# Kernel tuning notes

Hardware: AMD Instinct MI355X
Metric: run time of the kernel (lower is better)

## Reference

```python
import jax, jax.numpy as jnp
import numpy as np

B, S, H = 2, 2048, 4096
NH, NKV, HD = 32, 8, 128
N_REP = NH // NKV
SCALING = HD ** -0.5


def rotate_half(x):
    x1, x2 = x[..., : HD // 2], x[..., HD // 2 :]
    return jnp.concatenate((-x2, x1), axis=-1)


def setup_inputs() -> dict:
    key = jax.random.key(0)
    ks = jax.random.split(key, 8)
    hidden_states = jax.random.normal(ks[0], (B, S, H), dtype=jnp.float32)
    # RoPE tables computed as in Llama (deterministic, realistic values)
    inv_freq = 1.0 / (10000.0 ** (jnp.arange(0, HD, 2, dtype=jnp.float32) / HD))
    t = jnp.arange(S, dtype=jnp.float32)
    freqs = jnp.einsum('s,d->sd', t, inv_freq)
    emb = jnp.concatenate((freqs, freqs), axis=-1)  # [S, HD]
    cos = jnp.broadcast_to(jnp.cos(emb)[None], (B, S, HD))
    sin = jnp.broadcast_to(jnp.sin(emb)[None], (B, S, HD))
    # additive causal mask [B,1,S,S]
    causal = jnp.where(jnp.tril(jnp.ones((S, S), dtype=bool)), 0.0, -1e9).astype(jnp.float32)
    attention_mask = jnp.broadcast_to(causal[None, None], (B, 1, S, S))
    std = 0.02
    Wq = jax.random.normal(ks[1], (NH * HD, H), dtype=jnp.float32) * std
    Wk = jax.random.normal(ks[2], (NKV * HD, H), dtype=jnp.float32) * std
    Wv = jax.random.normal(ks[3], (NKV * HD, H), dtype=jnp.float32) * std
    Wo = jax.random.normal(ks[4], (H, NH * HD), dtype=jnp.float32) * std
    return dict(hidden_states=hidden_states, cos=cos, sin=sin,
                attention_mask=attention_mask, Wq=Wq, Wk=Wk, Wv=Wv, Wo=Wo)


def reference(hidden_states, cos, sin, attention_mask, Wq, Wk, Wv, Wo):
    b, s, _ = hidden_states.shape
    # projections (torch Linear: x @ W.T), split into heads -> [B, nH, S, HD]
    q = (hidden_states @ Wq.T).reshape(b, s, NH, HD).transpose(0, 2, 1, 3)
    k = (hidden_states @ Wk.T).reshape(b, s, NKV, HD).transpose(0, 2, 1, 3)
    v = (hidden_states @ Wv.T).reshape(b, s, NKV, HD).transpose(0, 2, 1, 3)
    # RoPE: cos/sin [B,S,HD] -> [B,1,S,HD]
    c, sn = cos[:, None], sin[:, None]
    q = q * c + rotate_half(q) * sn
    k = k * c + rotate_half(k) * sn
    # GQA: repeat kv heads
    k = jnp.repeat(k, N_REP, axis=1)
    v = jnp.repeat(v, N_REP, axis=1)
    scores = jnp.einsum('bhqd,bhkd->bhqk', q, k) * SCALING + attention_mask
    attn = jax.nn.softmax(scores.astype(jnp.float32), axis=-1).astype(q.dtype)
    out = jnp.einsum('bhqk,bhkd->bhqd', attn, v)
    out = out.transpose(0, 2, 1, 3).reshape(b, s, NH * HD)
    return out @ Wo.T
```

## Files before the change

kernel.cpp:

```cpp
#include <hip/hip_runtime.h>
#include <stdint.h>

typedef unsigned short u16;
typedef __attribute__((ext_vector_type(8))) short short8;
typedef __attribute__((ext_vector_type(4))) float f32x4;
typedef __attribute__((ext_vector_type(16))) float f32x16;
typedef __attribute__((ext_vector_type(4))) u16 u16x4;

static constexpr float SCALE = 0.08838834764831845f;
static constexpr float QSCALE = 0.12752459769642898f;

__device__ __forceinline__ u16 f2bf(float f) {
    union { float f; unsigned u; } x; x.f = f;
    unsigned r = x.u + 0x7fffu + ((x.u >> 16) & 1u);
    return (u16)(r >> 16);
}
__device__ __forceinline__ float bf2f(u16 b) {
    union { unsigned u; float f; } x; x.u = ((unsigned)b) << 16;
    return x.f;
}
__device__ __forceinline__ unsigned cvt_pk_bf16(float lo, float hi_) {
    unsigned r;
    asm("v_cvt_pk_bf16_f32 %0, %1, %2" : "=v"(r) : "v"(lo), "v"(hi_));
    return r;
}

__global__ __launch_bounds__(256) void convert5_kernel(const float* __restrict__ s0, const float* __restrict__ s1,
                                                       const float* __restrict__ s2, const float* __restrict__ s3,
                                                       const float* __restrict__ s4,
                                                       u16* __restrict__ d0, u16* __restrict__ d1,
                                                       u16* __restrict__ d2, u16* __restrict__ d3,
                                                       u16* __restrict__ d4) {
    const int V0 = 4194304, V1 = 8388608, V2 = 9437184, V3 = 10485760, V4 = 14680064;
    const int stride = gridDim.x * blockDim.x;
    for (int i = blockIdx.x * blockDim.x + threadIdx.x; i < V4; i += stride) {
        const float* sp; u16* dp; int off;
        if (i < V0)      { sp = s0; dp = d0; off = i; }
        else if (i < V1) { sp = s1; dp = d1; off = i - V0; }
        else if (i < V2) { sp = s2; dp = d2; off = i - V1; }
        else if (i < V3) { sp = s3; dp = d3; off = i - V2; }
        else             { sp = s4; dp = d4; off = i - V3; }
        float4 v = *reinterpret_cast<const float4*>(sp + (size_t)off * 4);
        u16x4 o;
        o.x = f2bf(v.x); o.y = f2bf(v.y); o.z = f2bf(v.z); o.w = f2bf(v.w);
        *reinterpret_cast<u16x4*>(dp + (size_t)off * 4) = o;
    }
}

__global__ __launch_bounds__(256) void gemm_kv(const u16* __restrict__ A,
                                               const u16* __restrict__ Bk,
                                               const u16* __restrict__ Bv,
                                               u16* __restrict__ Ck,
                                               u16* __restrict__ Cvt) {
    constexpr int K = 4096, N = 1024, BK = 64;
    __shared__ u16 sA[128 * BK];
    __shared__ u16 sB[128 * BK];
    const int tid = threadIdx.x;
    const int wid = tid >> 6, lane = tid & 63;
    const int lrow = lane & 15, lgrp = lane >> 4;

    int bid = blockIdx.x;
    { const int cpx = 512 >> 3; bid = (bid & 7) * cpx + (bid >> 3); }
    const bool isV = bid >= 256;
    const int b2 = bid & 255;
    const int row0 = (b2 >> 3) * 128, col0 = (b2 & 7) * 128;
    const u16* __restrict__ B = isV ? Bv : Bk;
    const int wr = (wid >> 1) * 64, wc = (wid & 1) * 64;

    f32x4 acc[4][4] = {};

    const int NT = K / BK;
    for (int kt = 0; kt < NT; ++kt) {
        const int k0 = kt * BK;
        __syncthreads();
        #pragma unroll
        for (int rnd = 0; rnd < 4; ++rnd) {
            const int eoff = (rnd * 256 + tid) * 8;
            const int r = eoff >> 6, c = eoff & 63;
            const int gc = c ^ ((r & 7) << 3);
            const int ldsoff = rnd * 2048 + wid * 512;
            __builtin_amdgcn_global_load_lds(
                (const __attribute__((address_space(1))) void*)(A + (size_t)(row0 + r) * K + k0 + gc),
                (__attribute__((address_space(3))) void*)(&sA[ldsoff]), 16, 0, 0);
            __builtin_amdgcn_global_load_lds(
                (const __attribute__((address_space(1))) void*)(B + (size_t)(col0 + r) * K + k0 + gc),
                (__attribute__((address_space(3))) void*)(&sB[ldsoff]), 16, 0, 0);
        }
        __syncthreads();
        #pragma unroll
        for (int kk = 0; kk < 2; ++kk) {
            const int koff = kk * 32 + lgrp * 8;
            short8 af[4], bfr[4];
            #pragma unroll
            for (int m = 0; m < 4; ++m) {
                const int rr = wr + m * 16 + lrow;
                af[m] = *(const short8*)&sA[rr * BK + (koff ^ ((rr & 7) << 3))];
            }
            #pragma unroll
            for (int n = 0; n < 4; ++n) {
                const int rr = wc + n * 16 + lrow;
                bfr[n] = *(const short8*)&sB[rr * BK + (koff ^ ((rr & 7) << 3))];
            }
            #pragma unroll
            for (int m = 0; m < 4; ++m)
                #pragma unroll
                for (int n = 0; n < 4; ++n)
                    acc[m][n] = __builtin_amdgcn_mfma_f32_16x16x32_bf16(af[m], bfr[n], acc[m][n], 0, 0, 0);
        }
    }

    const int orow = row0 + wr + lgrp * 4;
    const int ocol = col0 + wc + lrow;
    if (!isV) {
        #pragma unroll
        for (int m = 0; m < 4; ++m)
            #pragma unroll
            for (int n = 0; n < 4; ++n)
                #pragma unroll
                for (int r = 0; r < 4; ++r)
                    Ck[(size_t)(orow + m * 16 + r) * N + ocol + n * 16] = f2bf(acc[m][n][r]);
    } else {
        #pragma unroll
        for (int m = 0; m < 4; ++m)
            #pragma unroll
            for (int n = 0; n < 4; ++n) {
                u16x4 pk;
                pk.x = f2bf(acc[m][n][0]); pk.y = f2bf(acc[m][n][1]);
                pk.z = f2bf(acc[m][n][2]); pk.w = f2bf(acc[m][n][3]);
                *(u16x4*)&Cvt[(size_t)(ocol + n * 16) * 4096 + orow + m * 16] = pk;
            }
    }
}

template<int OUT_MODE>
__global__ __launch_bounds__(512, 1) void gemm256v5(const u16* __restrict__ A,
                                                    const u16* __restrict__ B,
                                                    void* __restrict__ Cv,
                                                    int M, int N, int K) {
    __shared__ u16 sA[2][2][256 * 32];
    __shared__ u16 sB[2][2][256 * 32];
    const int tid = threadIdx.x;
    const int wid = tid >> 6, lane = tid & 63;
    const int lrow = lane & 15, lgrp = lane >> 4;

    const int nbn = N >> 8;
    const int total = (M >> 8) * nbn;
    int bid = blockIdx.x;
    if ((total & 7) == 0) { const int cpx = total >> 3; bid = (bid & 7) * cpx + (bid >> 3); }
    const int row0 = (bid / nbn) * 256, col0 = (bid % nbn) * 256;
    const int wr = (wid >> 2) * 128, wc = (wid & 3) * 64;

    f32x4 acc[8][4] = {};

    const int rS0 = wid * 32 + (lane >> 2);
    const int uS = lane & 3;

    auto stageA = [&](int nb, int kt, int kkh) {
        const int k0 = kt * 64 + kkh * 32;
        #pragma unroll
        for (int g = 0; g < 2; ++g) {
            const int r = rS0 + g * 16;
            const int cs = k0 + ((uS ^ ((r >> 1) & 3)) << 3);
            __builtin_amdgcn_global_load_lds(
                (const __attribute__((address_space(1))) void*)(A + (size_t)(row0 + r) * K + cs),
                (__attribute__((address_space(3))) void*)(&sA[nb][kkh][(wid * 32 + g * 16) * 32]), 16, 0, 0);
        }
    };
    auto stageB = [&](int nb, int kt, int kkh) {
        const int k0 = kt * 64 + kkh * 32;
        #pragma unroll
        for (int g = 0; g < 2; ++g) {
            const int r = rS0 + g * 16;
            const int cs = k0 + ((uS ^ ((r >> 1) & 3)) << 3);
            __builtin_amdgcn_global_load_lds(
                (const __attribute__((address_space(1))) void*)(B + (size_t)(col0 + r) * K + cs),
                (__attribute__((address_space(3))) void*)(&sB[nb][kkh][(wid * 32 + g * 16) * 32]), 16, 0, 0);
        }
    };

    auto rdA = [&](int buf, int kkh, int fr) -> short8 {
        const int r = wr + fr * 16 + lrow;
        return *(const short8*)&sA[buf][kkh][r * 32 + ((lgrp ^ ((r >> 1) & 3)) << 3)];
    };
    auto rdB = [&](int buf, int kkh, int fc) -> short8 {
        const int r = wc + fc * 16 + lrow;
        return *(const short8*)&sB[buf][kkh][r * 32 + ((lgrp ^ ((r >> 1) & 3)) << 3)];
    };

    const int NK = K >> 6;
    stageA(0, 0, 0); stageB(0, 0, 0); stageA(0, 0, 1); stageB(0, 0, 1);
    asm volatile("s_waitcnt vmcnt(4)" ::: "memory");
    __builtin_amdgcn_s_barrier();
    __builtin_amdgcn_sched_barrier(0);

    short8 a0[4], b0[4], a1[4], a2[4], b1[4], a3[4];
    #pragma unroll
    for (int fr = 0; fr < 4; ++fr) a0[fr] = rdA(0, 0, fr);
    #pragma unroll
    for (int fc = 0; fc < 4; ++fc) b0[fc] = rdB(0, 0, fc);
    __builtin_amdgcn_sched_barrier(0);

    for (int kt = 0; kt < NK; ++kt) {
        const int buf = kt & 1, nb = buf ^ 1;
        const bool st = (kt + 1 < NK);

        #pragma unroll
        for (int fr = 0; fr < 4; ++fr) a1[fr] = rdA(buf, 0, fr + 4);
        if (st) stageA(nb, kt + 1, 0);
        asm volatile("s_waitcnt lgkmcnt(4)" ::: "memory");
        __builtin_amdgcn_sched_barrier(0);
        __builtin_amdgcn_s_setprio(1);
        #pragma unroll
        for (int fr = 0; fr < 4; ++fr)
            #pragma unroll
            for (int fc = 0; fc < 4; ++fc)
                acc[fr][fc] = __builtin_amdgcn_mfma_f32_16x16x32_bf16(a0[fr], b0[fc], acc[fr][fc], 0, 0, 0);
        __builtin_amdgcn_s_setprio(0);
        __builtin_amdgcn_sched_barrier(0);

        if (st) stageB(nb, kt + 1, 0);
        asm volatile("s_waitcnt lgkmcnt(0)" ::: "memory");
        __builtin_amdgcn_sched_barrier(0);
        if (st) { asm volatile("s_waitcnt vmcnt(4)" ::: "memory"); }
        else    { asm volatile("s_waitcnt vmcnt(0)" ::: "memory"); }
        __builtin_amdgcn_s_barrier();
        __builtin_amdgcn_sched_barrier(0);
        #pragma unroll
        for (int fr = 0; fr < 4; ++fr) a2[fr] = rdA(buf, 1, fr);
        #pragma unroll
        for (int fc = 0; fc < 4; ++fc) b1[fc] = rdB(buf, 1, fc);
        __builtin_amdgcn_sched_barrier(0);
        __builtin_amdgcn_s_setprio(1);
        #pragma unroll
        for (int fr = 0; fr < 4; ++fr)
            #pragma unroll
            for (int fc = 0; fc < 4; ++fc)
                acc[fr + 4][fc] = __builtin_amdgcn_mfma_f32_16x16x32_bf16(a1[fr], b0[fc], acc[fr + 4][fc], 0, 0, 0);
        __builtin_amdgcn_s_setprio(0);
        __builtin_amdgcn_sched_barrier(0);

        #pragma unroll
        for (int fr = 0; fr < 4; ++fr) a3[fr] = rdA(buf, 1, fr + 4);
        if (st) stageA(nb, kt + 1, 1);
        asm volatile("s_waitcnt lgkmcnt(4)" ::: "memory");
        __builtin_amdgcn_sched_barrier(0);
        __builtin_amdgcn_s_setprio(1);
        #pragma unroll
        for (int fr = 0; fr < 4; ++fr)
            #pragma unroll
            for (int fc = 0; fc < 4; ++fc)
                acc[fr][fc] = __builtin_amdgcn_mfma_f32_16x16x32_bf16(a2[fr], b1[fc], acc[fr][fc], 0, 0, 0);
        __builtin_amdgcn_s_setprio(0);
        __builtin_amdgcn_sched_barrier(0);

        if (st) stageB(nb, kt + 1, 1);
        asm volatile("s_waitcnt lgkmcnt(0)" ::: "memory");
        __builtin_amdgcn_sched_barrier(0);
        if (st) { asm volatile("s_waitcnt vmcnt(4)" ::: "memory"); }
        __builtin_amdgcn_s_barrier();
        __builtin_amdgcn_sched_barrier(0);
        if (st) {
            #pragma unroll
            for (int fr = 0; fr < 4; ++fr) a0[fr] = rdA(nb, 0, fr);
            #pragma unroll
            for (int fc = 0; fc < 4; ++fc) b0[fc] = rdB(nb, 0, fc);
        }
        __builtin_amdgcn_sched_barrier(0);
        __builtin_amdgcn_s_setprio(1);
        #pragma unroll
        for (int fr = 0; fr < 4; ++fr)
            #pragma unroll
            for (int fc = 0; fc < 4; ++fc)
                acc[fr + 4][fc] = __builtin_amdgcn_mfma_f32_16x16x32_bf16(a3[fr], b1[fc], acc[fr + 4][fc], 0, 0, 0);
        __builtin_amdgcn_s_setprio(0);
        __builtin_amdgcn_sched_barrier(0);
    }

    const int orow = row0 + wr + lgrp * 4;
    const int ocol = col0 + wc + lrow;
    if (OUT_MODE == 2) {
        float* C = (float*)Cv;
        #pragma unroll
        for (int m = 0; m < 8; ++m)
            #pragma unroll
            for (int n = 0; n < 4; ++n)
                #pragma unroll
                for (int r = 0; r < 4; ++r)
                    C[(size_t)(orow + m * 16 + r) * N + ocol + n * 16] = acc[m][n][r];
    } else {
        u16* C = (u16*)Cv;
        #pragma unroll
        for (int m = 0; m < 8; ++m)
            #pragma unroll
            for (int n = 0; n < 4; ++n)
                #pragma unroll
                for (int r = 0; r < 4; ++r)
                    C[(size_t)(orow + m * 16 + r) * N + ocol + n * 16] = f2bf(acc[m][n][r]);
    }
}

template<int NHEADS>
__global__ __launch_bounds__(256) void rope_kernel(u16* __restrict__ X,
                                                   const float* __restrict__ cosb,
                                                   const float* __restrict__ sinb,
                                                   float scale) {
    constexpr int LH = (NHEADS == 32) ? 5 : 3;
    const int total = 2 * 2048 * NHEADS * 64;
    const int stride = gridDim.x * blockDim.x;
    for (int i = blockIdx.x * blockDim.x + threadIdx.x; i < total; i += stride) {
        const int d = i & 63;
        const int h = (i >> 6) & (NHEADS - 1);
        const int rs = i >> (6 + LH);
        const size_t base = (size_t)rs * (NHEADS * 128) + h * 128 + d;
        const float c = cosb[rs * 128 + d] * scale;
        const float sn = sinb[rs * 128 + d] * scale;
        const float x1 = bf2f(X[base]);
        const float x2 = bf2f(X[base + 64]);
        X[base] = f2bf(x1 * c - x2 * sn);
        X[base + 64] = f2bf(x2 * c + x1 * sn);
    }
}

__global__ __launch_bounds__(512, 2) void attn_kernel(const u16* __restrict__ Q,
                                                      const u16* __restrict__ K,
                                                      const u16* __restrict__ Vt,
                                                      u16* __restrict__ AO,
                                                      const float* __restrict__ cosp,
                                                      const float* __restrict__ sinp) {
    __shared__ u16 sK[2][64 * 128];
    __shared__ u16 sV[2][128 * 64];
    const int tid = threadIdx.x;
    const int wid = tid >> 6, lane = tid & 63;
    const int l31 = lane & 31, hi = lane >> 5;

    const int gg = blockIdx.x >> 6;
    const int bx = (gg < 4) ? gg : 11 - gg;
    const int rem = blockIdx.x & 63;
    const int h = rem >> 1;
    const int b = rem & 1;
    const int hkv = h >> 2;
    const int rs0 = b * 2048;
    const int q0 = bx * 256;
    const int qw = q0 + wid * 32;
    const int q_lane = qw + l31;

    short8 qf[8];
    {
        const u16* qb = Q + (size_t)(rs0 + q_lane) * 4096 + h * 128 + hi * 8;
        #pragma unroll
        for (int f = 0; f < 8; ++f) qf[f] = *(const short8*)(qb + f * 16);
        const float* cb = cosp + (size_t)(rs0 + q_lane) * 128 + hi * 8;
        const float* sb = sinp + (size_t)(rs0 + q_lane) * 128 + hi * 8;
        #pragma unroll
        for (int f = 0; f < 4; ++f) {
            float4 c0 = *(const float4*)(cb + f * 16);
            float4 c1 = *(const float4*)(cb + f * 16 + 4);
            float4 s0 = *(const float4*)(sb + f * 16);
            float4 s1 = *(const float4*)(sb + f * 16 + 4);
            const float cc[8] = {c0.x, c0.y, c0.z, c0.w, c1.x, c1.y, c1.z, c1.w};
            const float ss[8] = {s0.x, s0.y, s0.z, s0.w, s1.x, s1.y, s1.z, s1.w};
            #pragma unroll
            for (int jj = 0; jj < 8; ++jj) {
                const float x1 = bf2f((u16)qf[f][jj]);
                const float x2 = bf2f((u16)qf[f + 4][jj]);
                qf[f][jj]     = (short)f2bf((x1 * cc[jj] - x2 * ss[jj]) * QSCALE);
                qf[f + 4][jj] = (short)f2bf((x2 * cc[jj] + x1 * ss[jj]) * QSCALE);
            }
        }
    }

    f32x16 accO[4] = {};
    float m_c = -1e30f, l_c = 0.f;

    auto stage = [&](int bf, int t) {
        const int kv0 = t * 64;
        #pragma unroll
        for (int rnd = 0; rnd < 2; ++rnd) {
            {
                const int e = rnd * 4096 + tid * 8;
                const int r = e >> 7, c = e & 127;
                const int cs = c ^ ((r & 15) << 3);
                __builtin_amdgcn_global_load_lds(
                    (const __attribute__((address_space(1))) void*)(K + (size_t)(rs0 + kv0 + r) * 1024 + hkv * 128 + cs),
                    (__attribute__((address_space(3))) void*)(&sK[bf][rnd * 4096 + wid * 512]), 16, 0, 0);
            }
            {
                const int e = rnd * 4096 + tid * 8;
                const int r = e >> 6, c = e & 63;
                const int cs = c ^ ((r & 7) << 3);
                __builtin_amdgcn_global_load_lds(
                    (const __attribute__((address_space(1))) void*)(Vt + (size_t)(hkv * 128 + r) * 4096 + rs0 + kv0 + cs),
                    (__attribute__((address_space(3))) void*)(&sV[bf][rnd * 4096 + wid * 512]), 16, 0, 0);
            }
        }
    };

    const int NT = 4 * (bx + 1);
    stage(0, 0);
    __syncthreads();
    int buf = 0;

    for (int t = 0; t < NT; ++t) {
        if (t + 1 < NT) stage(buf ^ 1, t + 1);
        const int kv0 = t * 64;

        if (kv0 <= qw + 31) {
            f32x16 sc[2] = {};
            #pragma unroll
            for (int f = 0; f < 8; ++f) {
                const int col = f * 16 + hi * 8;
                const int r0 = l31, r1 = 32 + l31;
                short8 k0 = *(const short8*)&sK[buf][r0 * 128 + (col ^ ((r0 & 15) << 3))];
                short8 k1 = *(const short8*)&sK[buf][r1 * 128 + (col ^ ((r1 & 15) << 3))];
                sc[0] = __builtin_amdgcn_mfma_f32_32x32x16_bf16(k0, qf[f], sc[0], 0, 0, 0);
                sc[1] = __builtin_amdgcn_mfma_f32_32x32x16_bf16(k1, qf[f], sc[1], 0, 0, 0);
            }

            if (kv0 + 63 > q_lane) {
                #pragma unroll
                for (int blk = 0; blk < 2; ++blk)
                    #pragma unroll
                    for (int r = 0; r < 16; ++r) {
                        const int kv_abs = kv0 + blk * 32 + ((r & 3) + 8 * (r >> 2) + 4 * hi);
                        if (kv_abs > q_lane) sc[blk][r] = -1e30f;
                    }
            }

            float mx = sc[0][0];
            #pragma unroll
            for (int blk = 0; blk < 2; ++blk)
                #pragma unroll
                for (int r = 0; r < 16; ++r) mx = fmaxf(mx, sc[blk][r]);
            mx = fmaxf(mx, __shfl_xor(mx, 32));

            if (!__all(mx <= m_c + 8.0f)) {
                const float sclf = __builtin_amdgcn_exp2f(m_c - mx);
                m_c = mx;
                l_c *= sclf;
                float sclq[16];
                #pragma unroll
                for (int r = 0; r < 16; ++r)
                    sclq[r] = __shfl(sclf, (r & 3) + 8 * (r >> 2) + 4 * hi);
                #pragma unroll
                for (int d4 = 0; d4 < 4; ++d4)
                    #pragma unroll
                    for (int r = 0; r < 16; ++r) accO[d4][r] *= sclq[r];
            }
            float ssum = 0.f;
            #pragma unroll
            for (int blk = 0; blk < 2; ++blk)
                #pragma unroll
                for (int r = 0; r < 16; ++r) {
                    const float p = __builtin_amdgcn_exp2f(sc[blk][r] - m_c);
                    sc[blk][r] = p;
                    ssum += p;
                }
            ssum += __shfl_xor(ssum, 32);
            l_c += ssum;

            #pragma unroll
            for (int blk = 0; blk < 2; ++blk) {
                #pragma unroll
                for (int tt = 0; tt < 2; ++tt) {
                    const unsigned cv00 = cvt_pk_bf16(sc[blk][8 * tt + 0], sc[blk][8 * tt + 1]);
                    const unsigned cv01 = cvt_pk_bf16(sc[blk][8 * tt + 2], sc[blk][8 * tt + 3]);
                    const unsigned cv10 = cvt_pk_bf16(sc[blk][8 * tt + 4], sc[blk][8 * tt + 5]);
                    const unsigned cv11 = cvt_pk_bf16(sc[blk][8 * tt + 6], sc[blk][8 * tt + 7]);
                    const unsigned s00 = __shfl_xor(cv00, 32);
                    const unsigned s01 = __shfl_xor(cv01, 32);
                    const unsigned s10 = __shfl_xor(cv10, 32);
                    const unsigned s11 = __shfl_xor(cv11, 32);
                    union { unsigned w[4]; short8 v; } pa;
                    pa.w[0] = hi ? s10 : cv00;
                    pa.w[1] = hi ? s11 : cv01;
                    pa.w[2] = hi ? cv10 : s00;
                    pa.w[3] = hi ? cv11 : s01;
                    const int kvb = blk * 32 + tt * 16 + hi * 8;
                    #pragma unroll
                    for (int d4 = 0; d4 < 4; ++d4) {
                        const int vr = d4 * 32 + l31;
                        short8 vf = *(const short8*)&sV[buf][vr * 64 + (kvb ^ ((vr & 7) << 3))];
                        accO[d4] = __builtin_amdgcn_mfma_f32_32x32x16_bf16(pa.v, vf, accO[d4], 0, 0, 0);
                    }
                }
            }
        }
        __syncthreads();
        buf ^= 1;
    }

    const float invl = 1.0f / l_c;
    float invq[16];
    #pragma unroll
    for (int r = 0; r < 16; ++r)
        invq[r] = __shfl(invl, (r & 3) + 8 * (r >> 2) + 4 * hi);
    #pragma unroll
    for (int d4 = 0; d4 < 4; ++d4)
        #pragma unroll
        for (int r = 0; r < 16; ++r) {
            const int q = qw + (r & 3) + 8 * (r >> 2) + 4 * hi;
            AO[(size_t)(rs0 + q) * 4096 + h * 128 + d4 * 32 + l31] = f2bf(accO[d4][r] * invq[r]);
        }
}

extern "C" void kernel_launch(void* const* d_in, const int* in_sizes, int n_in,
                              void* d_out, int out_size, void* d_ws, size_t ws_size,
                              hipStream_t stream) {
    const float* hs   = (const float*)d_in[0];
    const float* cosp = (const float*)d_in[1];
    const float* sinp = (const float*)d_in[2];
    const float* Wq = (const float*)d_in[4];
    const float* Wk = (const float*)d_in[5];
    const float* Wv = (const float*)d_in[6];
    const float* Wo = (const float*)d_in[7];

    u16* Xb = (u16*)d_out;
    u16* Qb = (u16*)d_out + 16777216;
    char* w = (char*)d_ws;
    u16* Wqb = (u16*)w; w += 33554432;
    u16* Wkb = (u16*)w; w += 8388608;
    u16* Wvb = (u16*)w; w += 8388608;
    u16* Wob = (u16*)w; w += 33554432;
    u16* Kb  = (u16*)w; w += 8388608;
    u16* Vtb = (u16*)w; w += 8388608;
    u16* AOb = (u16*)w; w += 33554432;

    convert5_kernel<<<4096, 256, 0, stream>>>(hs, Wq, Wk, Wv, Wo, Xb, Wqb, Wkb, Wvb, Wob);

    gemm256v5<0><<<256, 512, 0, stream>>>(Xb, Wqb, Qb, 4096, 4096, 4096);
    gemm_kv<<<512, 256, 0, stream>>>(Xb, Wkb, Wvb, Kb, Vtb);

    rope_kernel<8><<<1024, 256, 0, stream>>>(Kb, cosp, sinp, 1.0f);

    attn_kernel<<<512, 512, 0, stream>>>(Qb, Kb, Vtb, AOb, cosp, sinp);

    gemm256v5<2><<<256, 512, 0, stream>>>(AOb, Wob, (float*)d_out, 4096, 4096, 4096);
}
```

Measured before the change: 502.4 us.

## Load K and V fragments directly from global memory, dropping LDS staging

The attention kernel no longer stages K and Vt tiles into double-buffered shared memory with async global-to-LDS loads and block barriers. Each wave now reads its MFMA operand fragments straight from global memory and skips fully masked tiles per wave with continue. This removes the LDS traffic, the barriers and the shared-memory footprint. In exchange, the 8 waves of a block each re-read the same K/V data through the cache with no software prefetch, so load latency is exposed.

```diff
diff --git a/kernel.cpp b/kernel.cpp
--- a/kernel.cpp
+++ b/kernel.cpp
@@ -327,8 +327,6 @@
                                                       u16* __restrict__ AO,
                                                       const float* __restrict__ cosp,
                                                       const float* __restrict__ sinp) {
-    __shared__ u16 sK[2][64 * 128];
-    __shared__ u16 sV[2][128 * 64];
     const int tid = threadIdx.x;
     const int wid = tid >> 6, lane = tid & 63;
     const int l31 = lane & 31, hi = lane >> 5;
@@ -372,121 +370,91 @@
     f32x16 accO[4] = {};
     float m_c = -1e30f, l_c = 0.f;
 
-    auto stage = [&](int bf, int t) {
+    const u16* __restrict__ Kb0 = K + (size_t)(rs0 + l31) * 1024 + hkv * 128 + hi * 8;
+    const u16* __restrict__ Kb1 = K + (size_t)(rs0 + 32 + l31) * 1024 + hkv * 128 + hi * 8;
+    const u16* __restrict__ Vb = Vt + (size_t)(hkv * 128 + l31) * 4096 + rs0 + hi * 8;
+
+    const int NT = 4 * (bx + 1);
+    for (int t = 0; t < NT; ++t) {
         const int kv0 = t * 64;
-        #pragma unroll
-        for (int rnd = 0; rnd < 2; ++rnd) {
-            {
-                const int e = rnd * 4096 + tid * 8;
-                const int r = e >> 7, c = e & 127;
-                const int cs = c ^ ((r & 15) << 3);
-                __builtin_amdgcn_global_load_lds(
-                    (const __attribute__((address_space(1))) void*)(K + (size_t)(rs0 + kv0 + r) * 1024 + hkv * 128 + cs),
-                    (__attribute__((address_space(3))) void*)(&sK[bf][rnd * 4096 + wid * 512]), 16, 0, 0);
+        if (kv0 > qw + 31) continue;
+
+        f32x16 sc[2] = {};
+        #pragma unroll
+        for (int f = 0; f < 8; ++f) {
+            short8 k0 = *(const short8*)(Kb0 + (size_t)kv0 * 1024 + f * 16);
+            short8 k1 = *(const short8*)(Kb1 + (size_t)kv0 * 1024 + f * 16);
+            sc[0] = __builtin_amdgcn_mfma_f32_32x32x16_bf16(k0, qf[f], sc[0], 0, 0, 0);
+            sc[1] = __builtin_amdgcn_mfma_f32_32x32x16_bf16(k1, qf[f], sc[1], 0, 0, 0);
+        }
+
+        if (kv0 + 63 > q_lane) {
+            #pragma unroll
+            for (int blk = 0; blk < 2; ++blk)
+                #pragma unroll
+                for (int r = 0; r < 16; ++r) {
+                    const int kv_abs = kv0 + blk * 32 + ((r & 3) + 8 * (r >> 2) + 4 * hi);
+                    if (kv_abs > q_lane) sc[blk][r] = -1e30f;
+                }
+        }
+
+        float mx = sc[0][0];
+        #pragma unroll
+        for (int blk = 0; blk < 2; ++blk)
+            #pragma unroll
+            for (int r = 0; r < 16; ++r) mx = fmaxf(mx, sc[blk][r]);
+        mx = fmaxf(mx, __shfl_xor(mx, 32));
+
+        if (!__all(mx <= m_c + 8.0f)) {
+            const float sclf = __builtin_amdgcn_exp2f(m_c - mx);
+            m_c = mx;
+            l_c *= sclf;
+            float sclq[16];
+            #pragma unroll
+            for (int r = 0; r < 16; ++r)
+                sclq[r] = __shfl(sclf, (r & 3) + 8 * (r >> 2) + 4 * hi);
+            #pragma unroll
+            for (int d4 = 0; d4 < 4; ++d4)
+                #pragma unroll
+                for (int r = 0; r < 16; ++r) accO[d4][r] *= sclq[r];
+        }
+        float ssum = 0.f;
+        #pragma unroll
+        for (int blk = 0; blk < 2; ++blk)
+            #pragma unroll
+            for (int r = 0; r < 16; ++r) {
+                const float p = __builtin_amdgcn_exp2f(sc[blk][r] - m_c);
+                sc[blk][r] = p;
+                ssum += p;
             }
-            {
-                const int e = rnd * 4096 + tid * 8;
-                const int r = e >> 6, c = e & 63;
-                const int cs = c ^ ((r & 7) << 3);
-                __builtin_amdgcn_global_load_lds(
-                    (const __attribute__((address_space(1))) void*)(Vt + (size_t)(hkv * 128 + r) * 4096 + rs0 + kv0 + cs),
-                    (__attribute__((address_space(3))) void*)(&sV[bf][rnd * 4096 + wid * 512]), 16, 0, 0);
-            }
-        }
-    };
-
-    const int NT = 4 * (bx + 1);
-    stage(0, 0);
-    __syncthreads();
-    int buf = 0;
-
-    for (int t = 0; t < NT; ++t) {
-        if (t + 1 < NT) stage(buf ^ 1, t + 1);
-        const int kv0 = t * 64;
-
-        if (kv0 <= qw + 31) {
-            f32x16 sc[2] = {};
-            #pragma unroll
-            for (int f = 0; f < 8; ++f) {
-                const int col = f * 16 + hi * 8;
-                const int r0 = l31, r1 = 32 + l31;
-                short8 k0 = *(const short8*)&sK[buf][r0 * 128 + (col ^ ((r0 & 15) << 3))];
-                short8 k1 = *(const short8*)&sK[buf][r1 * 128 + (col ^ ((r1 & 15) << 3))];
-                sc[0] = __builtin_amdgcn_mfma_f32_32x32x16_bf16(k0, qf[f], sc[0], 0, 0, 0);
-                sc[1] = __builtin_amdgcn_mfma_f32_32x32x16_bf16(k1, qf[f], sc[1], 0, 0, 0);
-            }
-
-            if (kv0 + 63 > q_lane) {
-                #pragma unroll
-                for (int blk = 0; blk < 2; ++blk)
-                    #pragma unroll
-                    for (int r = 0; r < 16; ++r) {
-                        const int kv_abs = kv0 + blk * 32 + ((r & 3) + 8 * (r >> 2) + 4 * hi);
-                        if (kv_abs > q_lane) sc[blk][r] = -1e30f;
-                    }
-            }
-
-            float mx = sc[0][0];
-            #pragma unroll
-            for (int blk = 0; blk < 2; ++blk)
-                #pragma unroll
-                for (int r = 0; r < 16; ++r) mx = fmaxf(mx, sc[blk][r]);
-            mx = fmaxf(mx, __shfl_xor(mx, 32));
-
-            if (!__all(mx <= m_c + 8.0f)) {
-                const float sclf = __builtin_amdgcn_exp2f(m_c - mx);
-                m_c = mx;
-                l_c *= sclf;
-                float sclq[16];
-                #pragma unroll
-                for (int r = 0; r < 16; ++r)
-                    sclq[r] = __shfl(sclf, (r & 3) + 8 * (r >> 2) + 4 * hi);
-                #pragma unroll
-                for (int d4 = 0; d4 < 4; ++d4)
-                    #pragma unroll
-                    for (int r = 0; r < 16; ++r) accO[d4][r] *= sclq[r];
-            }
-            float ssum = 0.f;
-            #pragma unroll
-            for (int blk = 0; blk < 2; ++blk)
-                #pragma unroll
-                for (int r = 0; r < 16; ++r) {
-                    const float p = __builtin_amdgcn_exp2f(sc[blk][r] - m_c);
-                    sc[blk][r] = p;
-                    ssum += p;
-                }
-            ssum += __shfl_xor(ssum, 32);
-            l_c += ssum;
-
-            #pragma unroll
-            for (int blk = 0; blk < 2; ++blk) {
-                #pragma unroll
-                for (int tt = 0; tt < 2; ++tt) {
-                    const unsigned cv00 = cvt_pk_bf16(sc[blk][8 * tt + 0], sc[blk][8 * tt + 1]);
-                    const unsigned cv01 = cvt_pk_bf16(sc[blk][8 * tt + 2], sc[blk][8 * tt + 3]);
-                    const unsigned cv10 = cvt_pk_bf16(sc[blk][8 * tt + 4], sc[blk][8 * tt + 5]);
-                    const unsigned cv11 = cvt_pk_bf16(sc[blk][8 * tt + 6], sc[blk][8 * tt + 7]);
-                    const unsigned s00 = __shfl_xor(cv00, 32);
-                    const unsigned s01 = __shfl_xor(cv01, 32);
-                    const unsigned s10 = __shfl_xor(cv10, 32);
-                    const unsigned s11 = __shfl_xor(cv11, 32);
-                    union { unsigned w[4]; short8 v; } pa;
-                    pa.w[0] = hi ? s10 : cv00;
-                    pa.w[1] = hi ? s11 : cv01;
-                    pa.w[2] = hi ? cv10 : s00;
-                    pa.w[3] = hi ? cv11 : s01;
-                    const int kvb = blk * 32 + tt * 16 + hi * 8;
-                    #pragma unroll
-                    for (int d4 = 0; d4 < 4; ++d4) {
-                        const int vr = d4 * 32 + l31;
-                        short8 vf = *(const short8*)&sV[buf][vr * 64 + (kvb ^ ((vr & 7) << 3))];
-                        accO[d4] = __builtin_amdgcn_mfma_f32_32x32x16_bf16(pa.v, vf, accO[d4], 0, 0, 0);
-                    }
+        ssum += __shfl_xor(ssum, 32);
+        l_c += ssum;
+
+        #pragma unroll
+        for (int blk = 0; blk < 2; ++blk) {
+            #pragma unroll
+            for (int tt = 0; tt < 2; ++tt) {
+                const unsigned cv00 = cvt_pk_bf16(sc[blk][8 * tt + 0], sc[blk][8 * tt + 1]);
+                const unsigned cv01 = cvt_pk_bf16(sc[blk][8 * tt + 2], sc[blk][8 * tt + 3]);
+                const unsigned cv10 = cvt_pk_bf16(sc[blk][8 * tt + 4], sc[blk][8 * tt + 5]);
+                const unsigned cv11 = cvt_pk_bf16(sc[blk][8 * tt + 6], sc[blk][8 * tt + 7]);
+                const unsigned s00 = __shfl_xor(cv00, 32);
+                const unsigned s01 = __shfl_xor(cv01, 32);
+                const unsigned s10 = __shfl_xor(cv10, 32);
+                const unsigned s11 = __shfl_xor(cv11, 32);
+                union { unsigned w[4]; short8 v; } pa;
+                pa.w[0] = hi ? s10 : cv00;
+                pa.w[1] = hi ? s11 : cv01;
+                pa.w[2] = hi ? cv10 : s00;
+                pa.w[3] = hi ? cv11 : s01;
+                const int kvc = kv0 + blk * 32 + tt * 16;
+                #pragma unroll
+                for (int d4 = 0; d4 < 4; ++d4) {
+                    short8 vf = *(const short8*)(Vb + (size_t)(d4 * 32) * 4096 + kvc);
+                    accO[d4] = __builtin_amdgcn_mfma_f32_32x32x16_bf16(pa.v, vf, accO[d4], 0, 0, 0);
                 }
             }
         }
-        __syncthreads();
-        buf ^= 1;
     }
 
     const float invl = 1.0f / l_c;
```

Measured after the change: 705.2 us. 40.4% more time.
